# Performance work log

Hardware: AMD Instinct MI355X
Metric: run time of the kernel (lower is better)

## Reference

```python
import jax, jax.numpy as jnp
import numpy as np

B, U, W = 64, 128, 128  # batch, input_units, window_size (output units == U)

def setup_inputs() -> dict:
    key = jax.random.key(0)
    k1, k2, k3 = jax.random.split(key, 3)
    return {
        "input_tensor": jax.random.normal(k1, (B, U), dtype=jnp.float32),
        "state": jax.random.normal(k2, (B, U, W), dtype=jnp.float32),
        "w": jax.random.normal(k3, (2 * U + 1, U), dtype=jnp.float32) * 0.05,
        "b": jnp.zeros((U,), dtype=jnp.float32),
    }

def reference(input_tensor, state, w, b):
    b_, u_, w_ = state.shape
    # state @ state_shift is exactly a left-shift along the window axis
    new_state = jnp.concatenate([state[:, :, 1:], input_tensor[:, :, None]], axis=-1)  # [B,U,W]
    # NOTE: original uses tf.reshape (NOT transpose) [B,U,W] -> [B,W,U]; we replicate that
    flip = new_state.reshape(b_, w_, u_)                      # [B,W,U]
    # h_i[b,i,j,:] = flip[b,j,:] (stacked on axis=1); h_j[b,i,j,:] = flip[b,i,:]
    dot = jnp.einsum('biu,bju->bij', flip, flip)              # h_i . h_j, [B,W,W]
    w_hi, w_hj, w_dot = w[:u_], w[u_:2 * u_], w[2 * u_]       # split concat-matmul
    sim = (jnp.einsum('bju,uv->bjv', flip, w_hi)[:, None, :, :]   # h_i part
           + jnp.einsum('biu,uv->biv', flip, w_hj)[:, :, None, :] # h_j part
           + dot[..., None] * w_dot + b)                          # [B,W,W,U]
    a = jax.nn.softmax(sim, axis=2)                           # softmax over axis=-2 (j)
    c = jnp.einsum('bju,biju->biu', flip, a)                  # sum_j h_i * a_ij
    return c[:, -1, :]                                        # c_last, [B,U]
```

## Files before the change

kernel.cpp:

```cpp
#include <hip/hip_runtime.h>
#include <hip/hip_bf16.h>

constexpr int Bx = 64, Ux = 128, Wx = 128;
constexpr int LDST = 136;
constexpr int LDWT = 136;

typedef __attribute__((ext_vector_type(8))) short s16x8;
typedef __attribute__((ext_vector_type(4))) short s16x4;
typedef __attribute__((ext_vector_type(4))) float fx4;

static __device__ __forceinline__ short f2b(float x) {
  union { float f; unsigned u; } c; c.f = x;
  unsigned r = c.u + 0x7fffu + ((c.u >> 16) & 1u);
  return (short)(r >> 16);
}
static __device__ __forceinline__ float b2f(short s) {
  union { unsigned u; float f; } c; c.u = ((unsigned)(unsigned short)s) << 16;
  return c.f;
}

__global__ __launch_bounds__(1024) void rsa_kernel(const float* __restrict__ input,
                                                   const float* __restrict__ state,
                                                   const float* __restrict__ w,
                                                   float* __restrict__ out) {
  __shared__ __align__(16) short st_s[Wx][LDST];
  __shared__ __align__(16) short wst[Wx][LDWT];
  __shared__ float colmax[4][128], colsum[4][128], ppart[4][128];
  __shared__ float w127_s[128], wdot_s[128];
  __shared__ float dpart[2];

  const int t = threadIdx.x;
  const int b = blockIdx.x;
  const float* stb = state + (size_t)b * Ux * Wx;
  const float* inb = input + (size_t)b * Ux;

#pragma unroll
  for (int i = 0; i < 4; ++i) {
    int F = i * 1024 + t;
    int j = F >> 5, k4 = (F & 31) * 4;
    float4 x = *reinterpret_cast<const float4*>(stb + (size_t)F * 4);
    s16x4 p = { f2b(x.x), f2b(x.y), f2b(x.z), f2b(x.w) };
    *reinterpret_cast<s16x4*>(&st_s[j][k4]) = p;
  }
  if (t < Wx) st_s[t][128] = f2b(inb[t]);
#pragma unroll
  for (int i = 0; i < 4; ++i) {
    int F = i * 1024 + t;
    if (F < 4064) {
      int r = F >> 5, v4 = (F & 31) * 4;
      float4 x = *reinterpret_cast<const float4*>(w + r * Ux + v4);
      wst[v4 + 0][r + 1] = f2b(x.x);
      wst[v4 + 1][r + 1] = f2b(x.y);
      wst[v4 + 2][r + 1] = f2b(x.z);
      wst[v4 + 3][r + 1] = f2b(x.w);
    }
  }
  if (t < Wx) { wst[t][0] = 0; w127_s[t] = w[127 * Ux + t]; }
  else if (t < 2 * Wx) wdot_s[t - Wx] = w[2 * Ux * Ux + (t - Wx)];
  if (t < Wx) {
    float x = (t < Wx - 1) ? stb[127 * Wx + t + 1] : inb[127];
    float p = x * x;
#pragma unroll
    for (int off = 32; off; off >>= 1) p += __shfl_down(p, off);
    if ((t & 63) == 0) dpart[t >> 6] = p;
  }
  __syncthreads();

  const int wv = t >> 6, l = t & 63, lc = l & 15, lg = l >> 4;
  const int wr = wv >> 2, wc = wv & 3;
  fx4 aH[2][2] = {};
  fx4 aD[2] = {};
#pragma unroll
  for (int kt = 0; kt < 4; ++kt) {
    const int ko = kt * 32 + lg * 8;
    s16x8 bd = *reinterpret_cast<const s16x8*>(&st_s[127][ko]);
    s16x8 b0 = *reinterpret_cast<const s16x8*>(&wst[wc * 32 + lc][ko]);
    s16x8 b1 = *reinterpret_cast<const s16x8*>(&wst[wc * 32 + 16 + lc][ko]);
#pragma unroll
    for (int jl = 0; jl < 2; ++jl) {
      s16x8 a = *reinterpret_cast<const s16x8*>(&st_s[wr * 32 + jl * 16 + lc][ko]);
      aH[jl][0] = __builtin_amdgcn_mfma_f32_16x16x32_bf16(a, b0, aH[jl][0], 0, 0, 0);
      aH[jl][1] = __builtin_amdgcn_mfma_f32_16x16x32_bf16(a, b1, aH[jl][1], 0, 0, 0);
      aD[jl]    = __builtin_amdgcn_mfma_f32_16x16x32_bf16(a, bd, aD[jl],    0, 0, 0);
    }
  }

  const float in127  = b2f(st_s[127][128]);
  const float st0127 = b2f(st_s[127][0]);
  const float d127   = dpart[0] + dpart[1];
  const float wd0 = wdot_s[wc * 32 + lc],      wd1 = wdot_s[wc * 32 + 16 + lc];
  const float w70 = w127_s[wc * 32 + lc],      w71 = w127_s[wc * 32 + 16 + lc];
  float sim[2][2][4];
#pragma unroll
  for (int jl = 0; jl < 2; ++jl) {
#pragma unroll
    for (int r = 0; r < 4; ++r) {
      const int row = wr * 32 + jl * 16 + lg * 4 + r;
      float st0 = b2f(st_s[row][0]);
      float inr = b2f(st_s[row][128]);
      float dotv = aD[jl][r] - st0 * st0127 + inr * in127;
      if (row == Wx - 1) dotv = d127;
      sim[jl][0][r] = aH[jl][0][r] + dotv * wd0 + inr * w70;
      sim[jl][1][r] = aH[jl][1][r] + dotv * wd1 + inr * w71;
    }
  }

  float m0 = -3.4e38f, m1 = -3.4e38f;
#pragma unroll
  for (int jl = 0; jl < 2; ++jl)
#pragma unroll
    for (int r = 0; r < 4; ++r) {
      m0 = fmaxf(m0, sim[jl][0][r]);
      m1 = fmaxf(m1, sim[jl][1][r]);
    }
  m0 = fmaxf(m0, __shfl_xor(m0, 16)); m0 = fmaxf(m0, __shfl_xor(m0, 32));
  m1 = fmaxf(m1, __shfl_xor(m1, 16)); m1 = fmaxf(m1, __shfl_xor(m1, 32));
  if (l < 16) { colmax[wr][wc * 32 + l] = m0; colmax[wr][wc * 32 + 16 + l] = m1; }
  __syncthreads();
  const float M0 = fmaxf(fmaxf(colmax[0][wc * 32 + lc], colmax[1][wc * 32 + lc]),
                         fmaxf(colmax[2][wc * 32 + lc], colmax[3][wc * 32 + lc]));
  const float M1 = fmaxf(fmaxf(colmax[0][wc * 32 + 16 + lc], colmax[1][wc * 32 + 16 + lc]),
                         fmaxf(colmax[2][wc * 32 + 16 + lc], colmax[3][wc * 32 + 16 + lc]));
  float s0 = 0.f, s1 = 0.f, p0 = 0.f, p1 = 0.f;
#pragma unroll
  for (int jl = 0; jl < 2; ++jl)
#pragma unroll
    for (int r = 0; r < 4; ++r) {
      const int row = wr * 32 + jl * 16 + lg * 4 + r;
      float e0 = __expf(sim[jl][0][r] - M0);
      float e1 = __expf(sim[jl][1][r] - M1);
      s0 += e0; s1 += e1;
      p0 = fmaf(b2f(st_s[row][wc * 32 + lc + 1]), e0, p0);
      p1 = fmaf(b2f(st_s[row][wc * 32 + 16 + lc + 1]), e1, p1);
    }
  s0 += __shfl_xor(s0, 16); s0 += __shfl_xor(s0, 32);
  s1 += __shfl_xor(s1, 16); s1 += __shfl_xor(s1, 32);
  p0 += __shfl_xor(p0, 16); p0 += __shfl_xor(p0, 32);
  p1 += __shfl_xor(p1, 16); p1 += __shfl_xor(p1, 32);
  if (l < 16) {
    colsum[wr][wc * 32 + l] = s0; colsum[wr][wc * 32 + 16 + l] = s1;
    ppart[wr][wc * 32 + l]  = p0; ppart[wr][wc * 32 + 16 + l]  = p1;
  }
  __syncthreads();

  if (wr == 0 && l < 16) {
#pragma unroll
    for (int vl = 0; vl < 2; ++vl) {
      const int gv = wc * 32 + vl * 16 + l;
      float S = colsum[0][gv] + colsum[1][gv] + colsum[2][gv] + colsum[3][gv];
      float P = ppart[0][gv] + ppart[1][gv] + ppart[2][gv] + ppart[3][gv];
      out[(size_t)b * Ux + gv] = P / S;
    }
  }
}

extern "C" void kernel_launch(void* const* d_in, const int* in_sizes, int n_in,
                              void* d_out, int out_size, void* d_ws, size_t ws_size,
                              hipStream_t stream) {
  const float* input = (const float*)d_in[0];
  const float* state = (const float*)d_in[1];
  const float* w     = (const float*)d_in[2];
  float* out = (float*)d_out;
  rsa_kernel<<<dim3(Bx), dim3(1024), 0, stream>>>(input, state, w, out);
}
```

Measured before the change: 67.97 us.

## Split output columns across four blocks per batch with 256-thread blocks

Each batch is now handled by four blocks of 256 threads, each computing 32 output units instead of one 1024-thread block computing all 128. The grid grows from 64 to 256 blocks, so more compute units are in use, and each block loads only its slice of the weight matrix. In exchange, every block redundantly loads and converts the whole per-batch state tile. The state load is also widened to 16 floats per thread with 16-byte shared stores.

```diff
diff --git a/kernel.cpp b/kernel.cpp
--- a/kernel.cpp
+++ b/kernel.cpp
@@ -2,11 +2,12 @@
 #include <hip/hip_bf16.h>
 
 constexpr int Bx = 64, Ux = 128, Wx = 128;
+constexpr int NS = 4;
+constexpr int VC = 32;
 constexpr int LDST = 136;
 constexpr int LDWT = 136;
 
 typedef __attribute__((ext_vector_type(8))) short s16x8;
-typedef __attribute__((ext_vector_type(4))) short s16x4;
 typedef __attribute__((ext_vector_type(4))) float fx4;
 
 static __device__ __forceinline__ short f2b(float x) {
@@ -19,44 +20,42 @@
   return c.f;
 }
 
-__global__ __launch_bounds__(1024) void rsa_kernel(const float* __restrict__ input,
-                                                   const float* __restrict__ state,
-                                                   const float* __restrict__ w,
-                                                   float* __restrict__ out) {
+__global__ __launch_bounds__(256) void rsa_kernel(const float* __restrict__ input,
+                                                  const float* __restrict__ state,
+                                                  const float* __restrict__ w,
+                                                  float* __restrict__ out) {
   __shared__ __align__(16) short st_s[Wx][LDST];
-  __shared__ __align__(16) short wst[Wx][LDWT];
-  __shared__ float colmax[4][128], colsum[4][128], ppart[4][128];
-  __shared__ float w127_s[128], wdot_s[128];
+  __shared__ __align__(16) short wst[VC][LDWT];
+  __shared__ float colmax[4][VC], colsum[4][VC], ppart[4][VC];
+  __shared__ float w127_s[VC], wdot_s[VC];
   __shared__ float dpart[2];
 
   const int t = threadIdx.x;
-  const int b = blockIdx.x;
+  const int s = blockIdx.x, b = blockIdx.y;
+  const int vb = s * VC;
   const float* stb = state + (size_t)b * Ux * Wx;
   const float* inb = input + (size_t)b * Ux;
 
 #pragma unroll
   for (int i = 0; i < 4; ++i) {
-    int F = i * 1024 + t;
-    int j = F >> 5, k4 = (F & 31) * 4;
-    float4 x = *reinterpret_cast<const float4*>(stb + (size_t)F * 4);
-    s16x4 p = { f2b(x.x), f2b(x.y), f2b(x.z), f2b(x.w) };
-    *reinterpret_cast<s16x4*>(&st_s[j][k4]) = p;
+    int g = i * 4096 + t * 16;
+    int j = g >> 7, k = g & 127;
+    const float4* src = reinterpret_cast<const float4*>(stb + g);
+    float4 x0 = src[0], x1 = src[1], x2 = src[2], x3 = src[3];
+    s16x8 p0 = { f2b(x0.x), f2b(x0.y), f2b(x0.z), f2b(x0.w),
+                 f2b(x1.x), f2b(x1.y), f2b(x1.z), f2b(x1.w) };
+    s16x8 p1 = { f2b(x2.x), f2b(x2.y), f2b(x2.z), f2b(x2.w),
+                 f2b(x3.x), f2b(x3.y), f2b(x3.z), f2b(x3.w) };
+    *reinterpret_cast<s16x8*>(&st_s[j][k])     = p0;
+    *reinterpret_cast<s16x8*>(&st_s[j][k + 8]) = p1;
   }
   if (t < Wx) st_s[t][128] = f2b(inb[t]);
-#pragma unroll
-  for (int i = 0; i < 4; ++i) {
-    int F = i * 1024 + t;
-    if (F < 4064) {
-      int r = F >> 5, v4 = (F & 31) * 4;
-      float4 x = *reinterpret_cast<const float4*>(w + r * Ux + v4);
-      wst[v4 + 0][r + 1] = f2b(x.x);
-      wst[v4 + 1][r + 1] = f2b(x.y);
-      wst[v4 + 2][r + 1] = f2b(x.z);
-      wst[v4 + 3][r + 1] = f2b(x.w);
-    }
+  for (int idx = t; idx < 127 * VC; idx += 256) {
+    int r = idx >> 5, v = idx & (VC - 1);
+    wst[v][r + 1] = f2b(w[r * Ux + vb + v]);
   }
-  if (t < Wx) { wst[t][0] = 0; w127_s[t] = w[127 * Ux + t]; }
-  else if (t < 2 * Wx) wdot_s[t - Wx] = w[2 * Ux * Ux + (t - Wx)];
+  if (t < VC) { wst[t][0] = 0; w127_s[t] = w[127 * Ux + vb + t]; }
+  else if (t < 2 * VC) wdot_s[t - VC] = w[2 * Ux * Ux + vb + (t - VC)];
   if (t < Wx) {
     float x = (t < Wx - 1) ? stb[127 * Wx + t + 1] : inb[127];
     float p = x * x;
@@ -67,18 +66,17 @@
   __syncthreads();
 
   const int wv = t >> 6, l = t & 63, lc = l & 15, lg = l >> 4;
-  const int wr = wv >> 2, wc = wv & 3;
   fx4 aH[2][2] = {};
   fx4 aD[2] = {};
 #pragma unroll
   for (int kt = 0; kt < 4; ++kt) {
     const int ko = kt * 32 + lg * 8;
     s16x8 bd = *reinterpret_cast<const s16x8*>(&st_s[127][ko]);
-    s16x8 b0 = *reinterpret_cast<const s16x8*>(&wst[wc * 32 + lc][ko]);
-    s16x8 b1 = *reinterpret_cast<const s16x8*>(&wst[wc * 32 + 16 + lc][ko]);
+    s16x8 b0 = *reinterpret_cast<const s16x8*>(&wst[lc][ko]);
+    s16x8 b1 = *reinterpret_cast<const s16x8*>(&wst[lc + 16][ko]);
 #pragma unroll
     for (int jl = 0; jl < 2; ++jl) {
-      s16x8 a = *reinterpret_cast<const s16x8*>(&st_s[wr * 32 + jl * 16 + lc][ko]);
+      s16x8 a = *reinterpret_cast<const s16x8*>(&st_s[wv * 32 + jl * 16 + lc][ko]);
       aH[jl][0] = __builtin_amdgcn_mfma_f32_16x16x32_bf16(a, b0, aH[jl][0], 0, 0, 0);
       aH[jl][1] = __builtin_amdgcn_mfma_f32_16x16x32_bf16(a, b1, aH[jl][1], 0, 0, 0);
       aD[jl]    = __builtin_amdgcn_mfma_f32_16x16x32_bf16(a, bd, aD[jl],    0, 0, 0);
@@ -88,14 +86,14 @@
   const float in127  = b2f(st_s[127][128]);
   const float st0127 = b2f(st_s[127][0]);
   const float d127   = dpart[0] + dpart[1];
-  const float wd0 = wdot_s[wc * 32 + lc],      wd1 = wdot_s[wc * 32 + 16 + lc];
-  const float w70 = w127_s[wc * 32 + lc],      w71 = w127_s[wc * 32 + 16 + lc];
+  const float wd0 = wdot_s[lc], wd1 = wdot_s[lc + 16];
+  const float w70 = w127_s[lc], w71 = w127_s[lc + 16];
   float sim[2][2][4];
 #pragma unroll
   for (int jl = 0; jl < 2; ++jl) {
 #pragma unroll
     for (int r = 0; r < 4; ++r) {
-      const int row = wr * 32 + jl * 16 + lg * 4 + r;
+      const int row = wv * 32 + jl * 16 + lg * 4 + r;
       float st0 = b2f(st_s[row][0]);
       float inr = b2f(st_s[row][128]);
       float dotv = aD[jl][r] - st0 * st0127 + inr * in127;
@@ -115,42 +113,38 @@
     }
   m0 = fmaxf(m0, __shfl_xor(m0, 16)); m0 = fmaxf(m0, __shfl_xor(m0, 32));
   m1 = fmaxf(m1, __shfl_xor(m1, 16)); m1 = fmaxf(m1, __shfl_xor(m1, 32));
-  if (l < 16) { colmax[wr][wc * 32 + l] = m0; colmax[wr][wc * 32 + 16 + l] = m1; }
+  if (l < 16) { colmax[wv][l] = m0; colmax[wv][16 + l] = m1; }
   __syncthreads();
-  const float M0 = fmaxf(fmaxf(colmax[0][wc * 32 + lc], colmax[1][wc * 32 + lc]),
-                         fmaxf(colmax[2][wc * 32 + lc], colmax[3][wc * 32 + lc]));
-  const float M1 = fmaxf(fmaxf(colmax[0][wc * 32 + 16 + lc], colmax[1][wc * 32 + 16 + lc]),
-                         fmaxf(colmax[2][wc * 32 + 16 + lc], colmax[3][wc * 32 + 16 + lc]));
+  const float M0 = fmaxf(fmaxf(colmax[0][lc], colmax[1][lc]),
+                         fmaxf(colmax[2][lc], colmax[3][lc]));
+  const float M1 = fmaxf(fmaxf(colmax[0][lc + 16], colmax[1][lc + 16]),
+                         fmaxf(colmax[2][lc + 16], colmax[3][lc + 16]));
   float s0 = 0.f, s1 = 0.f, p0 = 0.f, p1 = 0.f;
 #pragma unroll
   for (int jl = 0; jl < 2; ++jl)
 #pragma unroll
     for (int r = 0; r < 4; ++r) {
-      const int row = wr * 32 + jl * 16 + lg * 4 + r;
+      const int row = wv * 32 + jl * 16 + lg * 4 + r;
       float e0 = __expf(sim[jl][0][r] - M0);
       float e1 = __expf(sim[jl][1][r] - M1);
       s0 += e0; s1 += e1;
-      p0 = fmaf(b2f(st_s[row][wc * 32 + lc + 1]), e0, p0);
-      p1 = fmaf(b2f(st_s[row][wc * 32 + 16 + lc + 1]), e1, p1);
+      p0 = fmaf(b2f(st_s[row][vb + lc + 1]), e0, p0);
+      p1 = fmaf(b2f(st_s[row][vb + lc + 17]), e1, p1);
     }
   s0 += __shfl_xor(s0, 16); s0 += __shfl_xor(s0, 32);
   s1 += __shfl_xor(s1, 16); s1 += __shfl_xor(s1, 32);
   p0 += __shfl_xor(p0, 16); p0 += __shfl_xor(p0, 32);
   p1 += __shfl_xor(p1, 16); p1 += __shfl_xor(p1, 32);
   if (l < 16) {
-    colsum[wr][wc * 32 + l] = s0; colsum[wr][wc * 32 + 16 + l] = s1;
-    ppart[wr][wc * 32 + l]  = p0; ppart[wr][wc * 32 + 16 + l]  = p1;
+    colsum[wv][l] = s0; colsum[wv][16 + l] = s1;
+    ppart[wv][l]  = p0; ppart[wv][16 + l]  = p1;
   }
   __syncthreads();
 
-  if (wr == 0 && l < 16) {
-#pragma unroll
-    for (int vl = 0; vl < 2; ++vl) {
-      const int gv = wc * 32 + vl * 16 + l;
-      float S = colsum[0][gv] + colsum[1][gv] + colsum[2][gv] + colsum[3][gv];
-      float P = ppart[0][gv] + ppart[1][gv] + ppart[2][gv] + ppart[3][gv];
-      out[(size_t)b * Ux + gv] = P / S;
-    }
+  if (wv == 0 && l < VC) {
+    float S = colsum[0][l] + colsum[1][l] + colsum[2][l] + colsum[3][l];
+    float P = ppart[0][l] + ppart[1][l] + ppart[2][l] + ppart[3][l];
+    out[(size_t)b * Ux + vb + l] = P / S;
   }
 }
 
@@ -161,5 +155,6 @@
   const float* state = (const float*)d_in[1];
   const float* w     = (const float*)d_in[2];
   float* out = (float*)d_out;
-  rsa_kernel<<<dim3(Bx), dim3(1024), 0, stream>>>(input, state, w, out);
+  dim3 grid(NS, Bx);
+  rsa_kernel<<<grid, dim3(256), 0, stream>>>(input, state, w, out);
 }
```

After: 66.57 us. -2.1%, faster.
